# Kernel tuning notes

Measured on AMD Instinct MI355X. Metric: run time of the kernel, lower is better.

The kernel has to match this reference:

```python
import jax, jax.numpy as jnp
import numpy as np

NINP, NHID, NOUT, DT = 128, 768, 128, 1.0
T, B = 256, 256


def setup_inputs() -> dict:
    key = jax.random.key(0)
    ks = jax.random.split(key, 9)
    std = 1.0 / np.sqrt(NHID)
    u = lambda k, shape: jax.random.uniform(k, shape, jnp.float32, -std, std)
    return {
        "input": jax.random.normal(ks[0], (T, B, NINP), jnp.float32),
        "W_inp": u(ks[1], (4 * NHID, NINP)),
        "b_inp": u(ks[2], (4 * NHID,)),
        "W_hid": u(ks[3], (3 * NHID, NHID)),
        "b_hid": u(ks[4], (3 * NHID,)),
        "W_z": u(ks[5], (NHID, NHID)),
        "b_z": u(ks[6], (NHID,)),
        "W_cls": jax.random.normal(ks[7], (NOUT, NHID), jnp.float32) * np.sqrt(2.0 / NHID),
        "b_cls": u(ks[8], (NOUT,)),
    }


def reference(input, W_inp, b_inp, W_hid, b_hid, W_z, b_z, W_cls, b_cls):
    # Precompute input projections for all timesteps: [T, B, 4*NHID]
    inp_proj = jnp.einsum('tbi,hi->tbh', input, W_inp) + b_inp

    def step(carry, xi):
        y, z = carry
        hid = y @ W_hid.T + b_hid                     # [B, 3*NHID]
        i_dt1, i_dt2, i_z, i_y = jnp.split(xi, 4, axis=1)
        h_dt1, h_dt2, h_y = jnp.split(hid, 3, axis=1)
        ms_dt_bar = DT * jax.nn.sigmoid(i_dt1 + h_dt1)
        ms_dt = DT * jax.nn.sigmoid(i_dt2 + h_dt2)
        z = (1.0 - ms_dt) * z + ms_dt * jnp.tanh(i_y + h_y)
        y = (1.0 - ms_dt_bar) * y + ms_dt_bar * jnp.tanh(z @ W_z.T + b_z + i_z)
        return (y, z), None

    y0 = jnp.zeros((input.shape[1], NHID), input.dtype)
    z0 = jnp.zeros_like(y0)
    (y, z), _ = jax.lax.scan(step, (y0, z0), inp_proj)
    return y @ W_cls.T + b_cls
```

## Files before the change

### kernel.cpp

```cpp
#include <hip/hip_runtime.h>
#include <stdint.h>


#define NINP 128
#define NHID 768
#define NOUT 128
#define T_STEPS 256
#define BATCH 256

#define NGRP 4
#define CBLK 48
#define NBLK (NGRP * CBLK)
#define NTHR 256
#define KH 24
#define KI 4

#define T_INP0 72
#define T_WZ0  88
#define NTILES 112

#define CHS 8192
#define SBUF 196608

typedef short bf16x8 __attribute__((ext_vector_type(8)));
typedef float f32x4 __attribute__((ext_vector_type(4)));
typedef unsigned uint32x4 __attribute__((ext_vector_type(4)));

__device__ __forceinline__ unsigned short f2b(float f) {
  union { float f; unsigned u; } x; x.f = f;
  return (unsigned short)((x.u + 0x7fffu + ((x.u >> 16) & 1u)) >> 16);
}
__device__ __forceinline__ float b2f(unsigned short h) {
  union { unsigned u; float f; } x; x.u = ((unsigned)h) << 16; return x.f;
}
__device__ __forceinline__ float fsig(float x) { return 1.0f / (1.0f + __expf(-x)); }
__device__ __forceinline__ float ftanh(float x) {
  float e = __expf(2.0f * x);
  return 1.0f - 2.0f / (e + 1.0f);
}

#define MFMA16(a, b, c) __builtin_amdgcn_mfma_f32_16x16x32_bf16(a, b, c, 0, 0, 0)

#define AL32(p) __hip_atomic_load((const unsigned*)(p), __ATOMIC_RELAXED, __HIP_MEMORY_SCOPE_AGENT)
#define AS32(p, v) __hip_atomic_store((unsigned*)(p), (v), __ATOMIC_RELAXED, __HIP_MEMORY_SCOPE_AGENT)
#define AS16(p, v) __hip_atomic_store((unsigned short*)(p), (v), __ATOMIC_RELAXED, __HIP_MEMORY_SCOPE_AGENT)

__device__ __forceinline__ void uld16(uint32x4* dst, const unsigned short* addr) {
  asm volatile("global_load_dwordx4 %0, %1, off sc0 sc1"
               : "=v"(*dst) : "v"(addr));
}
#define WAITV(N) do { \
  asm volatile("s_waitcnt vmcnt(" #N ")" ::: "memory"); \
  __builtin_amdgcn_sched_barrier(0); } while (0)

__device__ __forceinline__ void split8(const float* p, bf16x8* hi, bf16x8* lo) {
  union { bf16x8 v; unsigned short s[8]; } H, L;
#pragma unroll
  for (int e = 0; e < 8; ++e) {
    float v = p[e];
    unsigned short h = f2b(v);
    H.s[e] = h;
    L.s[e] = f2b(v - b2f(h));
  }
  *hi = H.v; *lo = L.v;
}

__global__ __launch_bounds__(NTHR, 1) void lem_kernel(
    const float* __restrict__ x,
    const float* __restrict__ W_inp,
    const float* __restrict__ b_inp,
    const float* __restrict__ W_hid,
    const float* __restrict__ b_hid,
    const float* __restrict__ W_z,
    const float* __restrict__ b_z,
    const float* __restrict__ W_cls,
    const float* __restrict__ b_cls,
    float* __restrict__ out,
    unsigned short* __restrict__ Y,
    unsigned short* __restrict__ Z,
    unsigned* __restrict__ flags)
{
  __shared__ unsigned short wlds[NTILES * 512];

  const int tid = threadIdx.x;
  const int l   = tid & 63;
  const int w   = tid >> 6;
  const int g   = blockIdx.x / CBLK;
  const int c   = blockIdx.x % CBLK;
  const int colbase = c * 16;
  const int lc  = l & 15;
  const int kg8 = (l >> 4) * 8;

  for (int idx = tid; idx < NTILES * 512; idx += NTHR) {
    int t = idx >> 9;
    int r = idx & 511;
    int ll = r >> 3;
    int e  = r & 7;
    int col16 = ll & 15;
    int kk = ((ll >> 4) * 8) + e;
    float v;
    if (t < T_INP0) {
      int seg = t / 24, kt = t % 24;
      v = W_hid[(size_t)(seg * NHID + colbase + col16) * NHID + kt * 32 + kk];
    } else if (t < T_WZ0) {
      int u = t - T_INP0; int seg = u >> 2, kt = u & 3;
      v = W_inp[(size_t)(seg * NHID + colbase + col16) * NINP + kt * 32 + kk];
    } else {
      int kt = t - T_WZ0;
      v = W_z[(size_t)(colbase + col16) * NHID + kt * 32 + kk];
    }
    wlds[idx] = f2b(v);
  }
  __syncthreads();

#define LDSB(t) (*(const bf16x8*)&wlds[((t) << 9) + (l << 3)])

  const int col  = colbase + lc;
  const int rt   = 4 * g + w;
  const int rowA = rt * 16 + lc;
  const int rowD = rt * 16 + (l >> 4) * 4;
  const int rtl  = rt * 512 + (l >> 4) * 128 + lc * 8;
  const float c1 = b_inp[col] + b_hid[col];
  const float c2 = b_inp[NHID + col] + b_hid[NHID + col];
  const float cy = b_inp[3 * NHID + col] + b_hid[2 * NHID + col];
  const float cz = b_inp[2 * NHID + col] + b_z[col];
  const int kts = col >> 5, kgs = (col >> 3) & 3, es = col & 7;
  const int r16b = (l >> 4) * 4;
  unsigned short* zs = Z + ((kts * 16 + rt) * 4 + kgs) * 128 + es;
  unsigned short* ys = Y + ((kts * 16 + rt) * 4 + kgs) * 128 + es;
  unsigned* gfA = flags + g * 128;
  unsigned* gfB = gfA + 64;

  f32x4 ai0{0,0,0,0}, ai1{0,0,0,0}, ai2{0,0,0,0}, ai3{0,0,0,0};
  {
    const float* xp0 = x + (size_t)rowA * NINP;
#pragma unroll
    for (int kt = 0; kt < KI; ++kt) {
      bf16x8 ah, al;
      split8(xp0 + kt * 32 + kg8, &ah, &al);
      ai0 = MFMA16(ah, LDSB(T_INP0 + 0 * 4 + kt), ai0);
      ai0 = MFMA16(al, LDSB(T_INP0 + 0 * 4 + kt), ai0);
      ai1 = MFMA16(ah, LDSB(T_INP0 + 1 * 4 + kt), ai1);
      ai1 = MFMA16(al, LDSB(T_INP0 + 1 * 4 + kt), ai1);
      ai2 = MFMA16(ah, LDSB(T_INP0 + 2 * 4 + kt), ai2);
      ai2 = MFMA16(al, LDSB(T_INP0 + 2 * 4 + kt), ai2);
      ai3 = MFMA16(ah, LDSB(T_INP0 + 3 * 4 + kt), ai3);
      ai3 = MFMA16(al, LDSB(T_INP0 + 3 * 4 + kt), ai3);
    }
  }

  f32x4 yloc{0,0,0,0}, zloc{0,0,0,0}, msb{0,0,0,0};

#define ISSUE(slot, jj) do { \
    uld16(&bufs[slot][0], pbase + (2 * (jj)) * CHS); \
    uld16(&bufs[slot][1], pbase + (2 * (jj) + 1) * CHS); } while (0)

  for (int s = 0; s < T_STEPS; ++s) {
    f32x4 h0{0,0,0,0}, h1{0,0,0,0}, h2{0,0,0,0};
    {
      const unsigned short* pbase = Y + rtl;
      uint32x4 bufs[6][2];
      ISSUE(0, 0); ISSUE(1, 1); ISSUE(2, 2); ISSUE(3, 3); ISSUE(4, 4);
#pragma unroll
      for (int j = 0; j < 12; ++j) {
        if (j <= 6) { ISSUE((j + 5) % 6, j + 5); WAITV(10); }
        else if (j == 7) { WAITV(8); }
        else if (j == 8) { WAITV(6); }
        else if (j == 9) { WAITV(4); }
        else if (j == 10) { WAITV(2); }
        else { WAITV(0); }
        const int sl = j % 6;
        bf16x8 a0 = __builtin_bit_cast(bf16x8, bufs[sl][0]);
        h0 = MFMA16(a0, LDSB(0 * 24 + 2 * j), h0);
        h1 = MFMA16(a0, LDSB(1 * 24 + 2 * j), h1);
        h2 = MFMA16(a0, LDSB(2 * 24 + 2 * j), h2);
        bf16x8 a1 = __builtin_bit_cast(bf16x8, bufs[sl][1]);
        h0 = MFMA16(a1, LDSB(0 * 24 + 2 * j + 1), h0);
        h1 = MFMA16(a1, LDSB(1 * 24 + 2 * j + 1), h1);
        h2 = MFMA16(a1, LDSB(2 * 24 + 2 * j + 1), h2);
      }
    }
#pragma unroll
    for (int i = 0; i < 4; ++i) {
      float a1 = fsig(ai0[i] + h0[i] + c1);
      float a2 = fsig(ai1[i] + h1[i] + c2);
      float gg = ftanh(ai3[i] + h2[i] + cy);
      float zn = (1.0f - a2) * zloc[i] + a2 * gg;
      zloc[i] = zn;
      msb[i] = a1;
      AS16(zs + (r16b + i) * 8, f2b(zn));
    }
    __syncthreads();
    if (tid == 0) AS32(&gfA[c], (unsigned)(s + 1));

    f32x4 ni0{0,0,0,0}, ni1{0,0,0,0}, ni2{0,0,0,0}, ni3{0,0,0,0};
    if (s + 1 < T_STEPS) {
      const float* xp = x + ((size_t)(s + 1) * BATCH + rowA) * NINP;
#pragma unroll
      for (int kt = 0; kt < KI; ++kt) {
        bf16x8 ah, al;
        split8(xp + kt * 32 + kg8, &ah, &al);
        ni0 = MFMA16(ah, LDSB(T_INP0 + 0 * 4 + kt), ni0);
        ni0 = MFMA16(al, LDSB(T_INP0 + 0 * 4 + kt), ni0);
        ni1 = MFMA16(ah, LDSB(T_INP0 + 1 * 4 + kt), ni1);
        ni1 = MFMA16(al, LDSB(T_INP0 + 1 * 4 + kt), ni1);
        ni2 = MFMA16(ah, LDSB(T_INP0 + 2 * 4 + kt), ni2);
        ni2 = MFMA16(al, LDSB(T_INP0 + 2 * 4 + kt), ni2);
        ni3 = MFMA16(ah, LDSB(T_INP0 + 3 * 4 + kt), ni3);
        ni3 = MFMA16(al, LDSB(T_INP0 + 3 * 4 + kt), ni3);
      }
    }
    if (w == 0) {
      const unsigned* fp = gfA + (l < CBLK ? l : 0);
      while (true) {
        unsigned v = AL32(fp);
        if (__all((l >= CBLK) || (v >= (unsigned)(s + 1)))) break;
        __builtin_amdgcn_s_sleep(1);
      }
    }
    __syncthreads();

    f32x4 az0{0,0,0,0}, az1{0,0,0,0};
    {
      const unsigned short* pbase = Z + rtl;
      uint32x4 bufs[6][2];
      ISSUE(0, 0); ISSUE(1, 1); ISSUE(2, 2); ISSUE(3, 3); ISSUE(4, 4);
#pragma unroll
      for (int j = 0; j < 12; ++j) {
        if (j <= 6) { ISSUE((j + 5) % 6, j + 5); WAITV(10); }
        else if (j == 7) { WAITV(8); }
        else if (j == 8) { WAITV(6); }
        else if (j == 9) { WAITV(4); }
        else if (j == 10) { WAITV(2); }
        else { WAITV(0); }
        const int sl = j % 6;
        bf16x8 a0 = __builtin_bit_cast(bf16x8, bufs[sl][0]);
        az0 = MFMA16(a0, LDSB(T_WZ0 + 2 * j), az0);
        bf16x8 a1 = __builtin_bit_cast(bf16x8, bufs[sl][1]);
        az1 = MFMA16(a1, LDSB(T_WZ0 + 2 * j + 1), az1);
      }
    }
#pragma unroll
    for (int i = 0; i < 4; ++i) {
      float tt = ftanh(az0[i] + az1[i] + ai2[i] + cz);
      float yn = (1.0f - msb[i]) * yloc[i] + msb[i] * tt;
      yloc[i] = yn;
      AS16(ys + (r16b + i) * 8, f2b(yn));
    }
    __syncthreads();
    if (tid == 0) AS32(&gfB[c], (unsigned)(s + 1));
    if (w == 0) {
      const unsigned* fp = gfB + (l < CBLK ? l : 0);
      while (true) {
        unsigned v = AL32(fp);
        if (__all((l >= CBLK) || (v >= (unsigned)(s + 1)))) break;
        __builtin_amdgcn_s_sleep(1);
      }
    }
    __syncthreads();

    ai0 = ni0; ai1 = ni1; ai2 = ni2; ai3 = ni3;
  }

  if (c < 8) {
    f32x4 ao0{0,0,0,0}, ao1{0,0,0,0};
    const unsigned short* pbase = Y + rtl;
    for (int kt = 0; kt < KH; kt += 2) {
      uint32x4 q0, q1;
      uld16(&q0, pbase + kt * CHS);
      uld16(&q1, pbase + (kt + 1) * CHS);
      bf16x8 bh0, bl0, bh1, bl1;
      split8(W_cls + (size_t)(colbase + lc) * NHID + kt * 32 + kg8, &bh0, &bl0);
      split8(W_cls + (size_t)(colbase + lc) * NHID + (kt + 1) * 32 + kg8, &bh1, &bl1);
      WAITV(0);
      bf16x8 a0 = __builtin_bit_cast(bf16x8, q0);
      ao0 = MFMA16(a0, bh0, ao0); ao0 = MFMA16(a0, bl0, ao0);
      bf16x8 a1 = __builtin_bit_cast(bf16x8, q1);
      ao1 = MFMA16(a1, bh1, ao1); ao1 = MFMA16(a1, bl1, ao1);
    }
    float bc = b_cls[colbase + lc];
#pragma unroll
    for (int i = 0; i < 4; ++i)
      out[(size_t)(rowD + i) * NOUT + colbase + lc] = ao0[i] + ao1[i] + bc;
  }
}

extern "C" void kernel_launch(void* const* d_in, const int* in_sizes, int n_in,
                              void* d_out, int out_size, void* d_ws, size_t ws_size,
                              hipStream_t stream) {
  (void)in_sizes; (void)n_in; (void)out_size; (void)ws_size;
  const float* x     = (const float*)d_in[0];
  const float* W_inp = (const float*)d_in[1];
  const float* b_inp = (const float*)d_in[2];
  const float* W_hid = (const float*)d_in[3];
  const float* b_hid = (const float*)d_in[4];
  const float* W_z   = (const float*)d_in[5];
  const float* b_z   = (const float*)d_in[6];
  const float* W_cls = (const float*)d_in[7];
  const float* b_cls = (const float*)d_in[8];

  unsigned short* Y = (unsigned short*)d_ws;
  unsigned short* Z = Y + SBUF;
  unsigned* flags = (unsigned*)((char*)d_ws + 2 * SBUF * sizeof(unsigned short));

  hipMemsetAsync(d_ws, 0, 2 * SBUF * sizeof(unsigned short) + NGRP * 128 * sizeof(unsigned), stream);

  lem_kernel<<<dim3(NBLK), dim3(NTHR), 0, stream>>>(
      x, W_inp, b_inp, W_hid, b_hid, W_z, b_z, W_cls, b_cls,
      (float*)d_out, Y, Z, flags);
}
```

Before: 2.274 ms.

## Halve persistent blocks, widen column tiles, stream W_z/W_inp from global

Each block now covers 32 hidden columns instead of 16, so the persistent grid drops from 192 to 96 blocks and fewer blocks take part in each grid-wide flag barrier. Only W_hid is kept in LDS. A new pre-kernel converts W_z and W_inp to bf16 tiles in the workspace, and the main loop streams them from global/L2 alongside the Z loads. Per-block MFMA work doubles and per-step global weight traffic is added, in exchange for less barrier contention and a smaller LDS footprint.

```diff
diff --git a/kernel.cpp b/kernel.cpp
--- a/kernel.cpp
+++ b/kernel.cpp
@@ -9,18 +9,19 @@
 #define BATCH 256
 
 #define NGRP 4
-#define CBLK 48
+#define CBLK 24
 #define NBLK (NGRP * CBLK)
 #define NTHR 256
 #define KH 24
 #define KI 4
 
-#define T_INP0 72
-#define T_WZ0  88
-#define NTILES 112
+#define NHTILES 144
 
 #define CHS 8192
 #define SBUF 196608
+
+#define WZ_TILES 1152
+#define WI_TILES 768
 
 typedef short bf16x8 __attribute__((ext_vector_type(8)));
 typedef float f32x4 __attribute__((ext_vector_type(4)));
@@ -47,6 +48,10 @@
 
 __device__ __forceinline__ void uld16(uint32x4* dst, const unsigned short* addr) {
   asm volatile("global_load_dwordx4 %0, %1, off sc0 sc1"
+               : "=v"(*dst) : "v"(addr));
+}
+__device__ __forceinline__ void cld16b(bf16x8* dst, const unsigned short* addr) {
+  asm volatile("global_load_dwordx4 %0, %1, off"
                : "=v"(*dst) : "v"(addr));
 }
 #define WAITV(N) do { \
@@ -65,105 +70,143 @@
   *hi = H.v; *lo = L.v;
 }
 
+__global__ __launch_bounds__(256) void conv_w(
+    const float* __restrict__ W_z, const float* __restrict__ W_inp,
+    unsigned short* __restrict__ Wz, unsigned short* __restrict__ Wi) {
+  int idx = blockIdx.x * 256 + threadIdx.x;
+  int t = idx >> 9, r = idx & 511;
+  int ll = r >> 3, e = r & 7;
+  int col16 = ll & 15;
+  int kk = ((ll >> 4) * 8) + e;
+  if (t < WZ_TILES) {
+    int kt = t % 24, n2 = (t / 24) & 1, c = t / 48;
+    Wz[idx] = f2b(W_z[(size_t)(c * 32 + n2 * 16 + col16) * NHID + kt * 32 + kk]);
+  } else {
+    int u = t - WZ_TILES;
+    int kt = u & 3, n2 = (u >> 2) & 1, seg = (u >> 3) & 3, c = u >> 5;
+    Wi[(size_t)u * 512 + r] =
+        f2b(W_inp[(size_t)(seg * NHID + c * 32 + n2 * 16 + col16) * NINP + kt * 32 + kk]);
+  }
+}
+
 __global__ __launch_bounds__(NTHR, 1) void lem_kernel(
     const float* __restrict__ x,
-    const float* __restrict__ W_inp,
     const float* __restrict__ b_inp,
     const float* __restrict__ W_hid,
     const float* __restrict__ b_hid,
-    const float* __restrict__ W_z,
     const float* __restrict__ b_z,
     const float* __restrict__ W_cls,
     const float* __restrict__ b_cls,
     float* __restrict__ out,
     unsigned short* __restrict__ Y,
     unsigned short* __restrict__ Z,
-    unsigned* __restrict__ flags)
+    unsigned* __restrict__ flags,
+    const unsigned short* __restrict__ Wz,
+    const unsigned short* __restrict__ Wi)
 {
-  __shared__ unsigned short wlds[NTILES * 512];
+  __shared__ unsigned short wlds[NHTILES * 512];
 
   const int tid = threadIdx.x;
   const int l   = tid & 63;
   const int w   = tid >> 6;
   const int g   = blockIdx.x / CBLK;
   const int c   = blockIdx.x % CBLK;
-  const int colbase = c * 16;
+  const int colbase = c * 32;
   const int lc  = l & 15;
   const int kg8 = (l >> 4) * 8;
 
-  for (int idx = tid; idx < NTILES * 512; idx += NTHR) {
+  for (int idx = tid; idx < NHTILES * 512; idx += NTHR) {
     int t = idx >> 9;
     int r = idx & 511;
-    int ll = r >> 3;
-    int e  = r & 7;
+    int ll = r >> 3, e = r & 7;
     int col16 = ll & 15;
     int kk = ((ll >> 4) * 8) + e;
-    float v;
-    if (t < T_INP0) {
-      int seg = t / 24, kt = t % 24;
-      v = W_hid[(size_t)(seg * NHID + colbase + col16) * NHID + kt * 32 + kk];
-    } else if (t < T_WZ0) {
-      int u = t - T_INP0; int seg = u >> 2, kt = u & 3;
-      v = W_inp[(size_t)(seg * NHID + colbase + col16) * NINP + kt * 32 + kk];
-    } else {
-      int kt = t - T_WZ0;
-      v = W_z[(size_t)(colbase + col16) * NHID + kt * 32 + kk];
-    }
-    wlds[idx] = f2b(v);
+    int kt = t % 24, sn = t / 24;
+    int seg = sn >> 1, n2 = sn & 1;
+    wlds[idx] = f2b(W_hid[(size_t)(seg * NHID + colbase + n2 * 16 + col16) * NHID + kt * 32 + kk]);
   }
   __syncthreads();
 
 #define LDSB(t) (*(const bf16x8*)&wlds[((t) << 9) + (l << 3)])
 
-  const int col  = colbase + lc;
   const int rt   = 4 * g + w;
   const int rowA = rt * 16 + lc;
   const int rowD = rt * 16 + (l >> 4) * 4;
   const int rtl  = rt * 512 + (l >> 4) * 128 + lc * 8;
-  const float c1 = b_inp[col] + b_hid[col];
-  const float c2 = b_inp[NHID + col] + b_hid[NHID + col];
-  const float cy = b_inp[3 * NHID + col] + b_hid[2 * NHID + col];
-  const float cz = b_inp[2 * NHID + col] + b_z[col];
-  const int kts = col >> 5, kgs = (col >> 3) & 3, es = col & 7;
   const int r16b = (l >> 4) * 4;
-  unsigned short* zs = Z + ((kts * 16 + rt) * 4 + kgs) * 128 + es;
-  unsigned short* ys = Y + ((kts * 16 + rt) * 4 + kgs) * 128 + es;
+
+  float c1[2], c2[2], cy[2], cz[2];
+  unsigned short *zs[2], *ys[2];
+#pragma unroll
+  for (int n2 = 0; n2 < 2; ++n2) {
+    int col = colbase + n2 * 16 + lc;
+    c1[n2] = b_inp[col] + b_hid[col];
+    c2[n2] = b_inp[NHID + col] + b_hid[NHID + col];
+    cy[n2] = b_inp[3 * NHID + col] + b_hid[2 * NHID + col];
+    cz[n2] = b_inp[2 * NHID + col] + b_z[col];
+    int kts = col >> 5, kgs = (col >> 3) & 3, es = col & 7;
+    zs[n2] = Z + ((kts * 16 + rt) * 4 + kgs) * 128 + es;
+    ys[n2] = Y + ((kts * 16 + rt) * 4 + kgs) * 128 + es;
+  }
   unsigned* gfA = flags + g * 128;
   unsigned* gfB = gfA + 64;
-
-  f32x4 ai0{0,0,0,0}, ai1{0,0,0,0}, ai2{0,0,0,0}, ai3{0,0,0,0};
+  const unsigned short* wzb = Wz + (size_t)(c * 48) * 512 + l * 8;
+  const unsigned short* wib = Wi + (size_t)(c * 32) * 512 + l * 8;
+
+  f32x4 ai[4][2];
+#pragma unroll
+  for (int sg = 0; sg < 4; ++sg)
+#pragma unroll
+    for (int n2 = 0; n2 < 2; ++n2) ai[sg][n2] = f32x4{0, 0, 0, 0};
   {
     const float* xp0 = x + (size_t)rowA * NINP;
 #pragma unroll
     for (int kt = 0; kt < KI; ++kt) {
       bf16x8 ah, al;
       split8(xp0 + kt * 32 + kg8, &ah, &al);
-      ai0 = MFMA16(ah, LDSB(T_INP0 + 0 * 4 + kt), ai0);
-      ai0 = MFMA16(al, LDSB(T_INP0 + 0 * 4 + kt), ai0);
-      ai1 = MFMA16(ah, LDSB(T_INP0 + 1 * 4 + kt), ai1);
-      ai1 = MFMA16(al, LDSB(T_INP0 + 1 * 4 + kt), ai1);
-      ai2 = MFMA16(ah, LDSB(T_INP0 + 2 * 4 + kt), ai2);
-      ai2 = MFMA16(al, LDSB(T_INP0 + 2 * 4 + kt), ai2);
-      ai3 = MFMA16(ah, LDSB(T_INP0 + 3 * 4 + kt), ai3);
-      ai3 = MFMA16(al, LDSB(T_INP0 + 3 * 4 + kt), ai3);
-    }
-  }
-
-  f32x4 yloc{0,0,0,0}, zloc{0,0,0,0}, msb{0,0,0,0};
-
-#define ISSUE(slot, jj) do { \
+#pragma unroll
+      for (int sg = 0; sg < 4; ++sg)
+#pragma unroll
+        for (int n2 = 0; n2 < 2; ++n2) {
+          bf16x8 bb = *(const bf16x8*)(wib + (((sg * 2 + n2) * 4) + kt) * 512);
+          ai[sg][n2] = MFMA16(ah, bb, ai[sg][n2]);
+          ai[sg][n2] = MFMA16(al, bb, ai[sg][n2]);
+        }
+    }
+  }
+
+  f32x4 yloc[2], zloc[2], msb[2];
+#pragma unroll
+  for (int n2 = 0; n2 < 2; ++n2) {
+    yloc[n2] = f32x4{0, 0, 0, 0};
+    zloc[n2] = f32x4{0, 0, 0, 0};
+  }
+
+#define ISSUE_A(slot, jj) do { \
     uld16(&bufs[slot][0], pbase + (2 * (jj)) * CHS); \
     uld16(&bufs[slot][1], pbase + (2 * (jj) + 1) * CHS); } while (0)
 
+#define ISSUE_B(slot, jj) do { \
+    uld16(&bufs[slot][0], pbase + (2 * (jj)) * CHS); \
+    uld16(&bufs[slot][1], pbase + (2 * (jj) + 1) * CHS); \
+    cld16b(&wzf[slot][0], wzb + (0 * 24 + 2 * (jj)) * 512); \
+    cld16b(&wzf[slot][1], wzb + (1 * 24 + 2 * (jj)) * 512); \
+    cld16b(&wzf[slot][2], wzb + (0 * 24 + 2 * (jj) + 1) * 512); \
+    cld16b(&wzf[slot][3], wzb + (1 * 24 + 2 * (jj) + 1) * 512); } while (0)
+
   for (int s = 0; s < T_STEPS; ++s) {
-    f32x4 h0{0,0,0,0}, h1{0,0,0,0}, h2{0,0,0,0};
+    f32x4 h[3][2];
+#pragma unroll
+    for (int sg = 0; sg < 3; ++sg)
+#pragma unroll
+      for (int n2 = 0; n2 < 2; ++n2) h[sg][n2] = f32x4{0, 0, 0, 0};
     {
       const unsigned short* pbase = Y + rtl;
       uint32x4 bufs[6][2];
-      ISSUE(0, 0); ISSUE(1, 1); ISSUE(2, 2); ISSUE(3, 3); ISSUE(4, 4);
+      ISSUE_A(0, 0); ISSUE_A(1, 1); ISSUE_A(2, 2); ISSUE_A(3, 3); ISSUE_A(4, 4);
 #pragma unroll
       for (int j = 0; j < 12; ++j) {
-        if (j <= 6) { ISSUE((j + 5) % 6, j + 5); WAITV(10); }
+        if (j <= 6) { ISSUE_A((j + 5) % 6, j + 5); WAITV(10); }
         else if (j == 7) { WAITV(8); }
         else if (j == 8) { WAITV(6); }
         else if (j == 9) { WAITV(4); }
@@ -171,43 +214,53 @@
         else { WAITV(0); }
         const int sl = j % 6;
         bf16x8 a0 = __builtin_bit_cast(bf16x8, bufs[sl][0]);
-        h0 = MFMA16(a0, LDSB(0 * 24 + 2 * j), h0);
-        h1 = MFMA16(a0, LDSB(1 * 24 + 2 * j), h1);
-        h2 = MFMA16(a0, LDSB(2 * 24 + 2 * j), h2);
+#pragma unroll
+        for (int sg = 0; sg < 3; ++sg)
+#pragma unroll
+          for (int n2 = 0; n2 < 2; ++n2)
+            h[sg][n2] = MFMA16(a0, LDSB((sg * 2 + n2) * 24 + 2 * j), h[sg][n2]);
         bf16x8 a1 = __builtin_bit_cast(bf16x8, bufs[sl][1]);
-        h0 = MFMA16(a1, LDSB(0 * 24 + 2 * j + 1), h0);
-        h1 = MFMA16(a1, LDSB(1 * 24 + 2 * j + 1), h1);
-        h2 = MFMA16(a1, LDSB(2 * 24 + 2 * j + 1), h2);
-      }
-    }
-#pragma unroll
-    for (int i = 0; i < 4; ++i) {
-      float a1 = fsig(ai0[i] + h0[i] + c1);
-      float a2 = fsig(ai1[i] + h1[i] + c2);
-      float gg = ftanh(ai3[i] + h2[i] + cy);
-      float zn = (1.0f - a2) * zloc[i] + a2 * gg;
-      zloc[i] = zn;
-      msb[i] = a1;
-      AS16(zs + (r16b + i) * 8, f2b(zn));
-    }
+#pragma unroll
+        for (int sg = 0; sg < 3; ++sg)
+#pragma unroll
+          for (int n2 = 0; n2 < 2; ++n2)
+            h[sg][n2] = MFMA16(a1, LDSB((sg * 2 + n2) * 24 + 2 * j + 1), h[sg][n2]);
+      }
+    }
+#pragma unroll
+    for (int n2 = 0; n2 < 2; ++n2)
+#pragma unroll
+      for (int i = 0; i < 4; ++i) {
+        float a1 = fsig(ai[0][n2][i] + h[0][n2][i] + c1[n2]);
+        float a2 = fsig(ai[1][n2][i] + h[1][n2][i] + c2[n2]);
+        float gg = ftanh(ai[3][n2][i] + h[2][n2][i] + cy[n2]);
+        float zn = (1.0f - a2) * zloc[n2][i] + a2 * gg;
+        zloc[n2][i] = zn;
+        msb[n2][i] = a1;
+        AS16(zs[n2] + (r16b + i) * 8, f2b(zn));
+      }
     __syncthreads();
     if (tid == 0) AS32(&gfA[c], (unsigned)(s + 1));
 
-    f32x4 ni0{0,0,0,0}, ni1{0,0,0,0}, ni2{0,0,0,0}, ni3{0,0,0,0};
+    f32x4 ni[4][2];
+#pragma unroll
+    for (int sg = 0; sg < 4; ++sg)
+#pragma unroll
+      for (int n2 = 0; n2 < 2; ++n2) ni[sg][n2] = f32x4{0, 0, 0, 0};
     if (s + 1 < T_STEPS) {
       const float* xp = x + ((size_t)(s + 1) * BATCH + rowA) * NINP;
 #pragma unroll
       for (int kt = 0; kt < KI; ++kt) {
         bf16x8 ah, al;
         split8(xp + kt * 32 + kg8, &ah, &al);
-        ni0 = MFMA16(ah, LDSB(T_INP0 + 0 * 4 + kt), ni0);
-        ni0 = MFMA16(al, LDSB(T_INP0 + 0 * 4 + kt), ni0);
-        ni1 = MFMA16(ah, LDSB(T_INP0 + 1 * 4 + kt), ni1);
-        ni1 = MFMA16(al, LDSB(T_INP0 + 1 * 4 + kt), ni1);
-        ni2 = MFMA16(ah, LDSB(T_INP0 + 2 * 4 + kt), ni2);
-        ni2 = MFMA16(al, LDSB(T_INP0 + 2 * 4 + kt), ni2);
-        ni3 = MFMA16(ah, LDSB(T_INP0 + 3 * 4 + kt), ni3);
-        ni3 = MFMA16(al, LDSB(T_INP0 + 3 * 4 + kt), ni3);
+#pragma unroll
+        for (int sg = 0; sg < 4; ++sg)
+#pragma unroll
+          for (int n2 = 0; n2 < 2; ++n2) {
+            bf16x8 bb = *(const bf16x8*)(wib + (((sg * 2 + n2) * 4) + kt) * 512);
+            ni[sg][n2] = MFMA16(ah, bb, ni[sg][n2]);
+            ni[sg][n2] = MFMA16(al, bb, ni[sg][n2]);
+          }
       }
     }
     if (w == 0) {
@@ -220,33 +273,39 @@
     }
     __syncthreads();
 
-    f32x4 az0{0,0,0,0}, az1{0,0,0,0};
+    f32x4 az[2];
+    az[0] = f32x4{0, 0, 0, 0}; az[1] = f32x4{0, 0, 0, 0};
     {
       const unsigned short* pbase = Z + rtl;
       uint32x4 bufs[6][2];
-      ISSUE(0, 0); ISSUE(1, 1); ISSUE(2, 2); ISSUE(3, 3); ISSUE(4, 4);
+      bf16x8 wzf[6][4];
+      ISSUE_B(0, 0); ISSUE_B(1, 1); ISSUE_B(2, 2); ISSUE_B(3, 3); ISSUE_B(4, 4);
 #pragma unroll
       for (int j = 0; j < 12; ++j) {
-        if (j <= 6) { ISSUE((j + 5) % 6, j + 5); WAITV(10); }
-        else if (j == 7) { WAITV(8); }
-        else if (j == 8) { WAITV(6); }
-        else if (j == 9) { WAITV(4); }
-        else if (j == 10) { WAITV(2); }
+        if (j <= 6) { ISSUE_B((j + 5) % 6, j + 5); WAITV(30); }
+        else if (j == 7) { WAITV(24); }
+        else if (j == 8) { WAITV(18); }
+        else if (j == 9) { WAITV(12); }
+        else if (j == 10) { WAITV(6); }
         else { WAITV(0); }
         const int sl = j % 6;
         bf16x8 a0 = __builtin_bit_cast(bf16x8, bufs[sl][0]);
-        az0 = MFMA16(a0, LDSB(T_WZ0 + 2 * j), az0);
+        az[0] = MFMA16(a0, wzf[sl][0], az[0]);
+        az[1] = MFMA16(a0, wzf[sl][1], az[1]);
         bf16x8 a1 = __builtin_bit_cast(bf16x8, bufs[sl][1]);
-        az1 = MFMA16(a1, LDSB(T_WZ0 + 2 * j + 1), az1);
-      }
-    }
-#pragma unroll
-    for (int i = 0; i < 4; ++i) {
-      float tt = ftanh(az0[i] + az1[i] + ai2[i] + cz);
-      float yn = (1.0f - msb[i]) * yloc[i] + msb[i] * tt;
-      yloc[i] = yn;
-      AS16(ys + (r16b + i) * 8, f2b(yn));
-    }
+        az[0] = MFMA16(a1, wzf[sl][2], az[0]);
+        az[1] = MFMA16(a1, wzf[sl][3], az[1]);
+      }
+    }
+#pragma unroll
+    for (int n2 = 0; n2 < 2; ++n2)
+#pragma unroll
+      for (int i = 0; i < 4; ++i) {
+        float tt = ftanh(az[n2][i] + ai[2][n2][i] + cz[n2]);
+        float yn = (1.0f - msb[n2][i]) * yloc[n2][i] + msb[n2][i] * tt;
+        yloc[n2][i] = yn;
+        AS16(ys[n2] + (r16b + i) * 8, f2b(yn));
+      }
     __syncthreads();
     if (tid == 0) AS32(&gfB[c], (unsigned)(s + 1));
     if (w == 0) {
@@ -259,29 +318,34 @@
     }
     __syncthreads();
 
-    ai0 = ni0; ai1 = ni1; ai2 = ni2; ai3 = ni3;
-  }
-
-  if (c < 8) {
-    f32x4 ao0{0,0,0,0}, ao1{0,0,0,0};
+#pragma unroll
+    for (int sg = 0; sg < 4; ++sg)
+#pragma unroll
+      for (int n2 = 0; n2 < 2; ++n2) ai[sg][n2] = ni[sg][n2];
+  }
+
+  if (c < 4) {
+    f32x4 ao[2];
+    ao[0] = f32x4{0, 0, 0, 0}; ao[1] = f32x4{0, 0, 0, 0};
     const unsigned short* pbase = Y + rtl;
-    for (int kt = 0; kt < KH; kt += 2) {
-      uint32x4 q0, q1;
-      uld16(&q0, pbase + kt * CHS);
-      uld16(&q1, pbase + (kt + 1) * CHS);
+    for (int kt = 0; kt < KH; ++kt) {
+      uint32x4 q;
+      uld16(&q, pbase + kt * CHS);
       bf16x8 bh0, bl0, bh1, bl1;
       split8(W_cls + (size_t)(colbase + lc) * NHID + kt * 32 + kg8, &bh0, &bl0);
-      split8(W_cls + (size_t)(colbase + lc) * NHID + (kt + 1) * 32 + kg8, &bh1, &bl1);
+      split8(W_cls + (size_t)(colbase + 16 + lc) * NHID + kt * 32 + kg8, &bh1, &bl1);
       WAITV(0);
-      bf16x8 a0 = __builtin_bit_cast(bf16x8, q0);
-      ao0 = MFMA16(a0, bh0, ao0); ao0 = MFMA16(a0, bl0, ao0);
-      bf16x8 a1 = __builtin_bit_cast(bf16x8, q1);
-      ao1 = MFMA16(a1, bh1, ao1); ao1 = MFMA16(a1, bl1, ao1);
-    }
-    float bc = b_cls[colbase + lc];
-#pragma unroll
-    for (int i = 0; i < 4; ++i)
-      out[(size_t)(rowD + i) * NOUT + colbase + lc] = ao0[i] + ao1[i] + bc;
+      bf16x8 a = __builtin_bit_cast(bf16x8, q);
+      ao[0] = MFMA16(a, bh0, ao[0]); ao[0] = MFMA16(a, bl0, ao[0]);
+      ao[1] = MFMA16(a, bh1, ao[1]); ao[1] = MFMA16(a, bl1, ao[1]);
+    }
+#pragma unroll
+    for (int n2 = 0; n2 < 2; ++n2) {
+      float bc = b_cls[colbase + n2 * 16 + lc];
+#pragma unroll
+      for (int i = 0; i < 4; ++i)
+        out[(size_t)(rowD + i) * NOUT + colbase + n2 * 16 + lc] = ao[n2][i] + bc;
+    }
   }
 }
 
@@ -301,11 +365,15 @@
 
   unsigned short* Y = (unsigned short*)d_ws;
   unsigned short* Z = Y + SBUF;
-  unsigned* flags = (unsigned*)((char*)d_ws + 2 * SBUF * sizeof(unsigned short));
+  unsigned* flags = (unsigned*)(Z + SBUF);
+  unsigned short* Wz = (unsigned short*)(flags + NGRP * 128);
+  unsigned short* Wi = Wz + (size_t)WZ_TILES * 512;
 
   hipMemsetAsync(d_ws, 0, 2 * SBUF * sizeof(unsigned short) + NGRP * 128 * sizeof(unsigned), stream);
 
+  conv_w<<<dim3((WZ_TILES + WI_TILES) * 2, 1, 1), dim3(256), 0, stream>>>(W_z, W_inp, Wz, Wi);
+
   lem_kernel<<<dim3(NBLK), dim3(NTHR), 0, stream>>>(
-      x, W_inp, b_inp, W_hid, b_hid, W_z, b_z, W_cls, b_cls,
-      (float*)d_out, Y, Z, flags);
-}
+      x, b_inp, W_hid, b_hid, b_z, W_cls, b_cls,
+      (float*)d_out, Y, Z, flags, Wz, Wi);
+}
```

Result: slower. 4.204 ms (+84.9%).
